# Performance work log

Hardware: AMD Instinct MI355X
Metric: run time of the kernel (lower is better)

The kernel has to match this reference:

```python
import jax, jax.numpy as jnp
import numpy as np

N, V, H, K = 65536, 200, 128, 32

def _corr_cols(a, B):
    # Pearson correlation between vector a [M] and each column of B [M, V]
    ac = a - a.mean()
    Bc = B - B.mean(axis=0)
    num = (ac[:, None] * Bc).sum(axis=0)
    den = jnp.sqrt((ac ** 2).sum() * (Bc ** 2).sum(axis=0))
    return jnp.nan_to_num(num / den, nan=0.0)

def _pairwise_features(tv, ti, cv, ci):
    # tv, ti: [N]; cv, ci: [N, V] -> features [V, 11]
    tvc = tv[:, None]
    both = (1.0 - ti)[:, None] * (1.0 - ci)
    n = both.sum(0) + 1e-8
    tmean = (tvc * both).sum(0) / n
    cmean = (cv * both).sum(0) / n
    tcent = (tvc - tmean) * both
    ccent = (cv - cmean) * both
    cov = (tcent * ccent).sum(0) / n
    tstd = jnp.sqrt((tcent ** 2).sum(0) / n + 1e-8)
    cstd = jnp.sqrt((ccent ** 2).sum(0) / n + 1e-8)
    corr = cov / (tstd * cstd + 1e-8)
    mi = -0.5 * jnp.log(1.0 - jnp.minimum(corr ** 2, 0.99) + 1e-8)
    tmin, tmax = tv.min(), tv.max()
    cmin, cmax = cv.min(0), cv.max(0)
    overlap = jnp.maximum(0.0, (jnp.minimum(tmax, cmax) - jnp.maximum(tmin, cmin)) / (jnp.maximum(tmax - tmin, cmax - cmin) + 1e-8))
    lag = _corr_cols(tv[1:], cv[:-1])       # corrcoef(candidate[:-1], target[1:])
    rev = _corr_cols(tv[:-1], cv[1:])       # corrcoef(target[:-1], candidate[1:])
    var_t = jnp.var(tv)
    coef = corr * jnp.std(tv) / (cv.std(0) + 1e-8)
    residual = tvc - coef * (cv - cv.mean(0))
    var_ratio = residual.var(0) / (var_t + 1e-8)
    intv = (ci > 0.5).astype(tv.dtype)
    t_int = (tvc * intv).sum(0) / (intv.sum(0) + 1e-8)
    t_no = (tvc * (1.0 - intv)).sum(0) / ((1.0 - intv).sum(0) + 1e-8)
    effect = jnp.abs(t_int - t_no)
    tr = jnp.argsort(jnp.argsort(tv)).astype(tv.dtype)
    cr = jnp.argsort(jnp.argsort(cv, axis=0), axis=0).astype(tv.dtype)
    rank_corr = _corr_cols(tr, cr)
    feats = jnp.stack([corr, jnp.abs(corr), corr ** 2, mi, overlap, effect,
                       rank_corr, jnp.sign(corr), lag, rev, var_ratio], axis=-1)
    return jnp.nan_to_num(feats, nan=0.0)

def _forward(target_embedding, node_embeddings, data, W_pair, b_pair, Wq, bq, Wk, bk,
             W1, b1, ln_scale, ln_offset, W2, b2, W3, b3, Wd, target_idx):
    n_vars = node_embeddings.shape[0]
    tv, ti = data[:, target_idx, 0], data[:, target_idx, 1]
    cv, ci = data[:, :, 0], data[:, :, 1]
    pf = _pairwise_features(tv, ti, cv, ci)                       # [V, 11]
    pf = jnp.where((jnp.arange(n_vars) == target_idx)[:, None], 0.0, pf)
    q = target_embedding @ Wq + bq                                # [K]
    k = node_embeddings @ Wk + bk + (pf @ W_pair + b_pair)        # [V, K]
    scores = (k @ q) / jnp.sqrt(jnp.asarray(float(K), dtype=q.dtype))
    te = jnp.broadcast_to(target_embedding, (n_vars, target_embedding.shape[0]))
    combined = jnp.concatenate([te, node_embeddings, pf * 10.0], axis=-1)  # [V, 2H+11]
    h = jax.nn.gelu(combined @ W1 + b1)
    mu = h.mean(-1, keepdims=True)
    var = ((h - mu) ** 2).mean(-1, keepdims=True)
    h = (h - mu) / jnp.sqrt(var + 1e-5) * ln_scale + ln_offset    # LayerNorm (haiku eps=1e-5)
    h = jax.nn.gelu(h @ W2 + b2)
    net = (h @ W3 + b3)[:, 0]
    direct = (pf[:, jnp.array([0, 8, 10])] @ Wd)[:, 0]
    return scores + net + 0.5 * direct

def setup_inputs():
    key = jax.random.key(0)
    ks = jax.random.split(key, 16)
    def vs_uniform(k, fan_in, shape):
        # hk.initializers.VarianceScaling(2.0, 'fan_in', 'uniform')
        lim = np.sqrt(6.0 / fan_in)
        return jax.random.uniform(k, shape, minval=-lim, maxval=lim, dtype=jnp.float32)
    vals = jax.random.normal(ks[0], (N, V), dtype=jnp.float32)
    intv = (jax.random.uniform(ks[1], (N, V)) < 0.1).astype(jnp.float32)
    data = jnp.stack([vals, intv, jnp.ones((N, V), jnp.float32)], axis=-1)  # [N, V, 3]
    return {
        'target_embedding': jax.random.normal(ks[2], (H,), dtype=jnp.float32),
        'node_embeddings': jax.random.normal(ks[3], (V, H), dtype=jnp.float32),
        'data': data,
        'W_pair': vs_uniform(ks[4], 11, (11, K)), 'b_pair': jnp.zeros((K,), jnp.float32),
        'Wq': vs_uniform(ks[5], H, (H, K)), 'bq': jnp.zeros((K,), jnp.float32),
        'Wk': vs_uniform(ks[6], H, (H, K)), 'bk': jnp.zeros((K,), jnp.float32),
        'W1': vs_uniform(ks[7], 2 * H + 11, (2 * H + 11, H)), 'b1': jnp.zeros((H,), jnp.float32),
        'ln_scale': jnp.ones((H,), jnp.float32), 'ln_offset': jnp.zeros((H,), jnp.float32),
        'W2': vs_uniform(ks[8], H, (H, H // 2)), 'b2': jnp.zeros((H // 2,), jnp.float32),
        'W3': vs_uniform(ks[9], H // 2, (H // 2, 1)), 'b3': jnp.zeros((1,), jnp.float32),
        'Wd': vs_uniform(ks[10], 3, (3, 1)),
        'target_idx': 0,
    }

def reference(target_embedding, node_embeddings, data, W_pair, b_pair, Wq, bq, Wk, bk,
              W1, b1, ln_scale, ln_offset, W2, b2, W3, b3, Wd, target_idx):
    return _forward(target_embedding, node_embeddings, data, W_pair, b_pair, Wq, bq, Wk, bk,
                    W1, b1, ln_scale, ln_offset, W2, b2, W3, b3, Wd, target_idx)
```

## Files before the change

### kernel.cpp

```cpp
#include <hip/hip_runtime.h>
#include <stdint.h>

#define N_ROWS 65536
#define NV 200
#define NH 128
#define NKD 32
#define NBKT 32768
#define NB2A 512

__device__ __forceinline__ uint32_t fkey(float x){
  uint32_t u = __float_as_uint(x);
  return (u & 0x80000000u) ? ~u : (u | 0x80000000u);
}

__global__ __launch_bounds__(256) void k_extract(
    const float* __restrict__ data, const int* __restrict__ tgt,
    float* __restrict__ tvArr, float* __restrict__ tiArr,
    unsigned int* __restrict__ histT, double* __restrict__ tvP){
  int i = blockIdx.x*256 + threadIdx.x;
  int tg = *tgt;
  float v  = data[(size_t)i*600 + tg*3 + 0];
  float ti = data[(size_t)i*600 + tg*3 + 1];
  tvArr[i] = v; tiArr[i] = ti;
  atomicAdd(&histT[fkey(v)>>17], 1u);
  double s = (double)v, ss = (double)v*(double)v;
  float mn = v, mx = v;
  for (int off=32; off; off>>=1){
    s  += __shfl_down(s,  off);
    ss += __shfl_down(ss, off);
    mn = fminf(mn, __shfl_down(mn, off));
    mx = fmaxf(mx, __shfl_down(mx, off));
  }
  __shared__ double sd[4][4];
  int w = threadIdx.x >> 6;
  if ((threadIdx.x & 63) == 0){ sd[w][0]=s; sd[w][1]=ss; sd[w][2]=mn; sd[w][3]=mx; }
  __syncthreads();
  if (threadIdx.x == 0){
    double S=0, SS=0, MN=sd[0][2], MX=sd[0][3];
    for (int q=0;q<4;q++){ S+=sd[q][0]; SS+=sd[q][1]; MN=fmin(MN,sd[q][2]); MX=fmax(MX,sd[q][3]); }
    double* p = tvP + (size_t)blockIdx.x*4;
    p[0]=S; p[1]=SS; p[2]=MN; p[3]=MX;
  }
}

__global__ __launch_bounds__(256) void k_comb_tv(const double* __restrict__ tvP,
                                                 double* __restrict__ tvStats){
  int t = threadIdx.x;
  double s = tvP[t*4+0], ss = tvP[t*4+1], mn = tvP[t*4+2], mx = tvP[t*4+3];
  for (int off=32; off; off>>=1){
    s  += __shfl_down(s,  off);
    ss += __shfl_down(ss, off);
    mn = fmin(mn, __shfl_down(mn, off));
    mx = fmax(mx, __shfl_down(mx, off));
  }
  __shared__ double sd[4][4];
  int w = t >> 6;
  if ((t & 63) == 0){ sd[w][0]=s; sd[w][1]=ss; sd[w][2]=mn; sd[w][3]=mx; }
  __syncthreads();
  if (t == 0){
    double S=0, SS=0, MN=sd[0][2], MX=sd[0][3];
    for (int q=0;q<4;q++){ S+=sd[q][0]; SS+=sd[q][1]; MN=fmin(MN,sd[q][2]); MX=fmax(MX,sd[q][3]); }
    tvStats[0]=S; tvStats[1]=SS; tvStats[2]=MN; tvStats[3]=MX;
  }
}

__global__ __launch_bounds__(256) void k_scan(unsigned int* __restrict__ histT){
  int t = threadIdx.x;
  unsigned int s = 0;
  unsigned int loc[128];
  #pragma unroll 8
  for (int k=0;k<128;k++){ loc[k] = histT[t*128+k]; s += loc[k]; }
  __shared__ unsigned int aux[256];
  aux[t] = s; __syncthreads();
  for (int off=1; off<256; off<<=1){
    unsigned int v = (t>=off) ? aux[t-off] : 0u;
    __syncthreads();
    aux[t] += v;
    __syncthreads();
  }
  unsigned int run = aux[t] - s;
  #pragma unroll 8
  for (int k=0;k<128;k++){
    unsigned int c = loc[k];
    float mid = (float)run + 0.5f*((float)c - 1.f);
    histT[t*128+k] = __float_as_uint(mid);
    run += c;
  }
}

__global__ __launch_bounds__(256) void k_trank(const float* __restrict__ tvArr,
                                               const unsigned int* __restrict__ histT,
                                               float* __restrict__ trArr){
  int i = blockIdx.x*256 + threadIdx.x;
  trArr[i] = __uint_as_float(histT[fkey(tvArr[i])>>17]);
}

__global__ __launch_bounds__(256, 2) void k_main(
    const float* __restrict__ data, const float* __restrict__ tvArr,
    const float* __restrict__ tiArr, uint16_t* __restrict__ bktT,
    double* __restrict__ colP, float* __restrict__ colMM){
  __shared__ float   cvS[64][201];
  __shared__ uint8_t ciS[64][204];
  __shared__ float   tvS[66];
  __shared__ float   tiS[64];
  int t = threadIdx.x, blk = blockIdx.x;
  double acc[13];
  #pragma unroll
  for (int s=0;s<13;s++) acc[s]=0.0;
  float cmin = 3.4e38f, cmax = -3.4e38f;

  for (int st=0; st<2; ++st){
    int i0 = blk*128 + st*64;
    const float4* rb = (const float4*)(data + (size_t)i0*600);
    #pragma unroll 2
    for (int k=0;k<38;k++){
      int f = t + k*256;
      if (f < 9600){
        float4 v = rb[f];
        int r  = f/150;
        int e4 = f - r*150;
        int m  = e4 % 3;
        int c0 = (4*e4)/3;
        if (m==0){ cvS[r][c0]=v.x; ciS[r][c0]=(uint8_t)(v.y>0.5f); cvS[r][c0+1]=v.w; }
        else if (m==1){ ciS[r][c0]=(uint8_t)(v.x>0.5f); cvS[r][c0+1]=v.z; ciS[r][c0+1]=(uint8_t)(v.w>0.5f); }
        else { cvS[r][c0+1]=v.y; ciS[r][c0+1]=(uint8_t)(v.z>0.5f); }
      }
    }
    if (t < 66){ int i = i0 - 1 + t; tvS[t] = (i>=0 && i<N_ROWS) ? tvArr[i] : 0.f; }
    else if (t >= 128 && t < 192){ tiS[t-128] = tiArr[i0 + (t-128)]; }
    __syncthreads();
    if (t < NV){
      float facc[13];
      #pragma unroll
      for (int s=0;s<13;s++) facc[s]=0.f;
      for (int r=0;r<64;r++){
        float cv = cvS[r][t];
        float ci = (float)ciS[r][t];
        float tv = tvS[r+1], tvm = tvS[r], tvp = tvS[r+2];
        float ti = tiS[r];
        float b  = (1.f-ti)*(1.f-ci);
        facc[0]+=cv;        facc[1]+=cv*cv;     facc[2]+=tv*cv;
        facc[3]+=ci;        facc[4]+=tv*ci;
        facc[5]+=b;         facc[6]+=tv*b;      facc[7]+=cv*b;
        facc[8]+=tv*cv*b;   facc[9]+=tv*tv*b;   facc[10]+=cv*cv*b;
        facc[11]+=tvp*cv;   facc[12]+=tvm*cv;
        cmin = fminf(cmin, cv); cmax = fmaxf(cmax, cv);
      }
      #pragma unroll
      for (int s=0;s<13;s++) acc[s] += (double)facc[s];
    }
    {
      int r = t & 63, cb = t >> 6;
      for (int cc=cb; cc<NV; cc+=4){
        float cv = cvS[r][cc];
        bktT[(size_t)cc*N_ROWS + i0 + r] = (uint16_t)(fkey(cv)>>17);
      }
    }
    __syncthreads();
  }
  if (t < NV){
    double* dst = colP + ((size_t)t*NB2A + blk)*16;
    #pragma unroll
    for (int s=0;s<13;s++) dst[s] = acc[s];
    float* mm = colMM + ((size_t)t*NB2A + blk)*2;
    mm[0]=cmin; mm[1]=cmax;
  }
}

__global__ __launch_bounds__(64) void k_comb_cols(const double* __restrict__ colP,
                                                  const float* __restrict__ colMM,
                                                  double* __restrict__ colStats){
  int j = blockIdx.x, t = threadIdx.x;
  double a[13];
  #pragma unroll
  for (int s=0;s<13;s++) a[s]=0.0;
  float mn = 3.4e38f, mx = -3.4e38f;
  for (int b=t; b<NB2A; b+=64){
    const double* p = colP + ((size_t)j*NB2A + b)*16;
    #pragma unroll
    for (int s=0;s<13;s++) a[s] += p[s];
    const float* m = colMM + ((size_t)j*NB2A + b)*2;
    mn = fminf(mn, m[0]); mx = fmaxf(mx, m[1]);
  }
  for (int off=32; off; off>>=1){
    #pragma unroll
    for (int s=0;s<13;s++) a[s] += __shfl_down(a[s], off);
    mn = fminf(mn, __shfl_down(mn, off));
    mx = fmaxf(mx, __shfl_down(mx, off));
  }
  if (t == 0){
    double* d = colStats + (size_t)j*16;
    #pragma unroll
    for (int s=0;s<13;s++) d[s] = a[s];
    d[13] = (double)mn; d[14] = (double)mx;
  }
}

__global__ __launch_bounds__(256) void k_rank(const uint16_t* __restrict__ bktT,
                                              const float* __restrict__ trArr,
                                              double* __restrict__ colStats){
  __shared__ unsigned int h[NBKT];
  __shared__ unsigned int aux[256];
  __shared__ double daux[4];
  int t = threadIdx.x, j = blockIdx.x;
  const uint16_t* col = bktT + (size_t)j*N_ROWS;
  for (int k=t; k<NBKT; k+=256) h[k]=0u;
  __syncthreads();
  for (int k=0;k<N_ROWS/256;k++){
    int b = (int)col[t + k*256];
    atomicAdd(&h[b], 1u);
  }
  __syncthreads();
  unsigned int s = 0;
  for (int k=0;k<128;k++) s += h[t*128+k];
  aux[t]=s; __syncthreads();
  for (int off=1; off<256; off<<=1){
    unsigned int v = (t>=off) ? aux[t-off] : 0u;
    __syncthreads();
    aux[t] += v;
    __syncthreads();
  }
  unsigned int run = aux[t] - s;
  for (int k=0;k<128;k++){
    unsigned int c = h[t*128+k];
    float mid = (float)run + 0.5f*((float)c - 1.f);
    h[t*128+k] = __float_as_uint(mid);
    run += c;
  }
  __syncthreads();
  double srr = 0.0;
  for (int k=0;k<N_ROWS/256;k++){
    int i = t + k*256;
    int b = (int)col[i];
    srr += (double)trArr[i] * (double)__uint_as_float(h[b]);
  }
  for (int off=32; off; off>>=1) srr += __shfl_down(srr, off);
  if ((t&63)==0) daux[t>>6] = srr;
  __syncthreads();
  if (t==0) colStats[(size_t)j*16 + 15] = daux[0]+daux[1]+daux[2]+daux[3];
}

__device__ __forceinline__ float gelu_t(float x){
  float x3 = x*x*x;
  return 0.5f*x*(1.f + tanhf(0.7978845608f*(x + 0.044715f*x3)));
}

__global__ __launch_bounds__(128) void k_head(
    const float* __restrict__ te, const float* __restrict__ ne, const float* __restrict__ data,
    const float* __restrict__ Wpair, const float* __restrict__ bpair,
    const float* __restrict__ Wq, const float* __restrict__ bq,
    const float* __restrict__ Wk, const float* __restrict__ bk,
    const float* __restrict__ W1, const float* __restrict__ b1,
    const float* __restrict__ lns, const float* __restrict__ lno,
    const float* __restrict__ W2, const float* __restrict__ b2,
    const float* __restrict__ W3, const float* __restrict__ b3,
    const float* __restrict__ Wd, const int* __restrict__ tgt,
    const double* __restrict__ colStats, const double* __restrict__ tvStats,
    const float* __restrict__ tvArr, float* __restrict__ out){
  int j = blockIdx.x, t = threadIdx.x;
  int tg = *tgt;
  const double* cs = colStats + (size_t)j*16;
  double S_c=cs[0], S_cc=cs[1], S_tc=cs[2], S_ci=cs[3], S_ti=cs[4], S_b=cs[5],
         S_tb=cs[6], S_cb=cs[7], S_tcb=cs[8], S_ttb=cs[9], S_ccb=cs[10], L=cs[11], R=cs[12];
  float cmin=(float)cs[13], cmax=(float)cs[14];
  double S_rr=cs[15];
  double S_t=tvStats[0], S_tt=tvStats[1];
  float tmin=(float)tvStats[2], tmax=(float)tvStats[3];
  float tv0=tvArr[0], tvN=tvArr[N_ROWS-1];
  float cv0=data[j*3], cvN=data[(size_t)(N_ROWS-1)*600 + j*3];
  const double Nd = (double)N_ROWS;
  double n = S_b + 1e-8;
  double tmean=S_tb/n, cmean=S_cb/n;
  double cov=(S_tcb - tmean*S_cb - cmean*S_tb + tmean*cmean*S_b)/n;
  double t2=S_ttb - 2.0*tmean*S_tb + tmean*tmean*S_b;
  double c2=S_ccb - 2.0*cmean*S_cb + cmean*cmean*S_b;
  double tstd=sqrt(t2/n + 1e-8), cstd=sqrt(c2/n + 1e-8);
  double corr = cov/(tstd*cstd + 1e-8);
  double mi = -0.5*log(1.0 - fmin(corr*corr, 0.99) + 1e-8);
  float ovn = fminf(tmax,cmax) - fmaxf(tmin,cmin);
  float ovd = fmaxf(tmax-tmin, cmax-cmin) + 1e-8f;
  float overlap = fmaxf(0.f, ovn/ovd);
  double M = Nd - 1.0;
  double Sa=S_t-(double)tv0, Saa=S_tt-(double)tv0*(double)tv0;
  double Sb2=S_c-(double)cvN, Sbb=S_cc-(double)cvN*(double)cvN;
  double lnum = L - Sa*Sb2/M;
  double lden2 = (Saa - Sa*Sa/M)*(Sbb - Sb2*Sb2/M);
  double lag = (lden2 > 0.0) ? lnum/sqrt(lden2) : 0.0;
  double Sa2=S_t-(double)tvN, Saa2=S_tt-(double)tvN*(double)tvN;
  double Sc2=S_c-(double)cv0, Scc2=S_cc-(double)cv0*(double)cv0;
  double rnum = R - Sa2*Sc2/M;
  double rden2 = (Saa2 - Sa2*Sa2/M)*(Scc2 - Sc2*Sc2/M);
  double rev = (rden2 > 0.0) ? rnum/sqrt(rden2) : 0.0;
  double var_t = S_tt/Nd - (S_t/Nd)*(S_t/Nd);
  double var_c = S_cc/Nd - (S_c/Nd)*(S_c/Nd);
  double coef = corr*sqrt(var_t)/(sqrt(var_c) + 1e-8);
  double covf = S_tc/Nd - (S_t/Nd)*(S_c/Nd);
  double var_res = var_t + coef*coef*var_c - 2.0*coef*covf;
  double var_ratio = var_res/(var_t + 1e-8);
  double t_int = S_ti/(S_ci + 1e-8);
  double t_no  = (S_t - S_ti)/((Nd - S_ci) + 1e-8);
  double effect = fabs(t_int - t_no);
  const double m_ = (Nd-1.0)*0.5;
  double rank_corr = (S_rr - Nd*m_*m_) / (Nd*(Nd*Nd-1.0)/12.0);
  float pf[11];
  pf[0]=(float)corr; pf[1]=(float)fabs(corr); pf[2]=(float)(corr*corr); pf[3]=(float)mi;
  pf[4]=overlap; pf[5]=(float)effect; pf[6]=(float)rank_corr;
  pf[7]=(float)((corr>0.0)-(corr<0.0)); pf[8]=(float)lag; pf[9]=(float)rev; pf[10]=(float)var_ratio;
  if (j == tg){
    #pragma unroll
    for (int q=0;q<11;q++) pf[q]=0.f;
  }
  const float* nej = ne + (size_t)j*NH;
  float h = b1[t];
  for (int e=0;e<NH;e++) h += te[e]*W1[e*NH + t];
  for (int e=0;e<NH;e++) h += nej[e]*W1[(NH+e)*NH + t];
  #pragma unroll
  for (int f=0;f<11;f++) h += 10.f*pf[f]*W1[(2*NH+f)*NH + t];
  h = gelu_t(h);
  __shared__ float redW[2];
  __shared__ float hnS[NH];
  __shared__ float h2S[64];
  float v = h;
  for (int off=32; off; off>>=1) v += __shfl_down(v, off);
  if ((t&63)==0) redW[t>>6]=v;
  __syncthreads();
  float mu = (redW[0]+redW[1])*(1.f/128.f);
  __syncthreads();
  float d = h - mu;
  v = d*d;
  for (int off=32; off; off>>=1) v += __shfl_down(v, off);
  if ((t&63)==0) redW[t>>6]=v;
  __syncthreads();
  float var = (redW[0]+redW[1])*(1.f/128.f);
  float hn = d/sqrtf(var + 1e-5f)*lns[t] + lno[t];
  hnS[t] = hn;
  __syncthreads();
  if (t < 64){
    float h2 = b2[t];
    for (int o=0;o<NH;o++) h2 += hnS[o]*W2[o*64 + t];
    h2S[t] = gelu_t(h2);
  }
  __syncthreads();
  float netv = 0.f, scv = 0.f;
  if (t < 64){
    float v2 = h2S[t]*W3[t];
    for (int off=32; off; off>>=1) v2 += __shfl_down(v2, off);
    if (t==0) netv = v2 + b3[0];
  }
  if (t < 32){
    float q = bq[t], k = bk[t] + bpair[t];
    for (int e=0;e<NH;e++){ q += te[e]*Wq[e*NKD + t]; k += nej[e]*Wk[e*NKD + t]; }
    #pragma unroll
    for (int f=0;f<11;f++) k += pf[f]*Wpair[f*NKD + t];
    float sc = k*q;
    for (int off=16; off; off>>=1) sc += __shfl_down(sc, off, 32);
    if (t==0) scv = sc/sqrtf(32.f);
  }
  if (t == 0){
    float direct = pf[0]*Wd[0] + pf[8]*Wd[1] + pf[10]*Wd[2];
    out[j] = scv + netv + 0.5f*direct;
  }
}

extern "C" void kernel_launch(void* const* d_in, const int* in_sizes, int n_in,
                              void* d_out, int out_size, void* d_ws, size_t ws_size,
                              hipStream_t stream) {
  const float* te    = (const float*)d_in[0];
  const float* ne    = (const float*)d_in[1];
  const float* data  = (const float*)d_in[2];
  const float* Wpair = (const float*)d_in[3];
  const float* bpair = (const float*)d_in[4];
  const float* Wq    = (const float*)d_in[5];
  const float* bq    = (const float*)d_in[6];
  const float* Wk    = (const float*)d_in[7];
  const float* bk    = (const float*)d_in[8];
  const float* W1    = (const float*)d_in[9];
  const float* b1    = (const float*)d_in[10];
  const float* lns   = (const float*)d_in[11];
  const float* lno   = (const float*)d_in[12];
  const float* W2    = (const float*)d_in[13];
  const float* b2    = (const float*)d_in[14];
  const float* W3    = (const float*)d_in[15];
  const float* b3    = (const float*)d_in[16];
  const float* Wd    = (const float*)d_in[17];
  const int*   tgt   = (const int*)d_in[18];
  float* out = (float*)d_out;

  char* ws = (char*)d_ws;
  size_t off = 0;
  auto alloc = [&](size_t bytes)->char*{
    char* p = ws + off;
    off = (off + bytes + 255) & ~(size_t)255;
    return p;
  };
  uint16_t*     bktT     = (uint16_t*)    alloc((size_t)NV*N_ROWS*2);
  float*        tvArr    = (float*)       alloc(N_ROWS*4);
  float*        tiArr    = (float*)       alloc(N_ROWS*4);
  float*        trArr    = (float*)       alloc(N_ROWS*4);
  unsigned int* histT    = (unsigned int*)alloc(NBKT*4);
  double*       tvP      = (double*)      alloc(256*4*8);
  double*       tvStats  = (double*)      alloc(4*8);
  double*       colP     = (double*)      alloc((size_t)NV*NB2A*16*8);
  float*        colMM    = (float*)       alloc((size_t)NV*NB2A*2*4);
  double*       colStats = (double*)      alloc((size_t)NV*16*8);
  if (off > ws_size) return;

  hipMemsetAsync(histT, 0, NBKT*4, stream);
  k_extract<<<dim3(N_ROWS/256), dim3(256), 0, stream>>>(data, tgt, tvArr, tiArr, histT, tvP);
  k_comb_tv<<<dim3(1), dim3(256), 0, stream>>>(tvP, tvStats);
  k_scan<<<dim3(1), dim3(256), 0, stream>>>(histT);
  k_trank<<<dim3(N_ROWS/256), dim3(256), 0, stream>>>(tvArr, histT, trArr);
  k_main<<<dim3(NB2A), dim3(256), 0, stream>>>(data, tvArr, tiArr, bktT, colP, colMM);
  k_comb_cols<<<dim3(NV), dim3(64), 0, stream>>>(colP, colMM, colStats);
  k_rank<<<dim3(NV), dim3(256), 0, stream>>>(bktT, trArr, colStats);
  k_head<<<dim3(NV), dim3(128), 0, stream>>>(te, ne, data, Wpair, bpair, Wq, bq, Wk, bk,
                                             W1, b1, lns, lno, W2, b2, W3, b3, Wd, tgt,
                                             colStats, tvStats, tvArr, out);
}
```

Before: 463.8 us.

## Shrink k_main stage tiles, widen rank/comb blocks, stage scan histogram in LDS

k_main now stages 32 rows per step instead of 64, which roughly halves LDS use, and requests 4 blocks per CU instead of 2 to raise occupancy. Per-block column partials are stored as floats, with min and max packed into the same record, which removes a separate buffer and halves the partial traffic. k_comb_cols uses 256 threads with a shared-memory cross-wave reduction. k_rank uses 512 threads with a padded histogram layout to reduce LDS bank conflicts, and k_scan stages the histogram through padded LDS instead of a per-thread register array. Storing partial sums as float risks some loss of precision, and the larger per-block LDS in k_rank limits it to one block per CU.

```diff
diff --git a/kernel.cpp b/kernel.cpp
--- a/kernel.cpp
+++ b/kernel.cpp
@@ -7,6 +7,7 @@
 #define NKD 32
 #define NBKT 32768
 #define NB2A 512
+#define ROWS_ST 32
 
 __device__ __forceinline__ uint32_t fkey(float x){
   uint32_t u = __float_as_uint(x);
@@ -65,12 +66,14 @@
 }
 
 __global__ __launch_bounds__(256) void k_scan(unsigned int* __restrict__ histT){
+  __shared__ unsigned int h[256*129];
+  __shared__ unsigned int aux[256];
   int t = threadIdx.x;
+  for (int idx=t; idx<NBKT; idx+=256) h[(idx>>7)*129 + (idx&127)] = histT[idx];
+  __syncthreads();
   unsigned int s = 0;
-  unsigned int loc[128];
   #pragma unroll 8
-  for (int k=0;k<128;k++){ loc[k] = histT[t*128+k]; s += loc[k]; }
-  __shared__ unsigned int aux[256];
+  for (int k=0;k<128;k++) s += h[t*129+k];
   aux[t] = s; __syncthreads();
   for (int off=1; off<256; off<<=1){
     unsigned int v = (t>=off) ? aux[t-off] : 0u;
@@ -81,11 +84,12 @@
   unsigned int run = aux[t] - s;
   #pragma unroll 8
   for (int k=0;k<128;k++){
-    unsigned int c = loc[k];
-    float mid = (float)run + 0.5f*((float)c - 1.f);
-    histT[t*128+k] = __float_as_uint(mid);
+    unsigned int c = h[t*129+k];
+    h[t*129+k] = __float_as_uint((float)run + 0.5f*((float)c - 1.f));
     run += c;
   }
+  __syncthreads();
+  for (int idx=t; idx<NBKT; idx+=256) histT[idx] = h[(idx>>7)*129 + (idx&127)];
 }
 
 __global__ __launch_bounds__(256) void k_trank(const float* __restrict__ tvArr,
@@ -95,27 +99,27 @@
   trArr[i] = __uint_as_float(histT[fkey(tvArr[i])>>17]);
 }
 
-__global__ __launch_bounds__(256, 2) void k_main(
+__global__ __launch_bounds__(256, 4) void k_main(
     const float* __restrict__ data, const float* __restrict__ tvArr,
     const float* __restrict__ tiArr, uint16_t* __restrict__ bktT,
-    double* __restrict__ colP, float* __restrict__ colMM){
-  __shared__ float   cvS[64][201];
-  __shared__ uint8_t ciS[64][204];
-  __shared__ float   tvS[66];
-  __shared__ float   tiS[64];
+    float* __restrict__ colP){
+  __shared__ float   cvS[ROWS_ST][201];
+  __shared__ uint8_t ciS[ROWS_ST][204];
+  __shared__ float   tvS[ROWS_ST+2];
+  __shared__ float   tiS[ROWS_ST];
   int t = threadIdx.x, blk = blockIdx.x;
   double acc[13];
   #pragma unroll
   for (int s=0;s<13;s++) acc[s]=0.0;
   float cmin = 3.4e38f, cmax = -3.4e38f;
 
-  for (int st=0; st<2; ++st){
-    int i0 = blk*128 + st*64;
+  for (int st=0; st<4; ++st){
+    int i0 = blk*128 + st*ROWS_ST;
     const float4* rb = (const float4*)(data + (size_t)i0*600);
     #pragma unroll 2
-    for (int k=0;k<38;k++){
+    for (int k=0;k<19;k++){
       int f = t + k*256;
-      if (f < 9600){
+      if (f < 4800){
         float4 v = rb[f];
         int r  = f/150;
         int e4 = f - r*150;
@@ -126,14 +130,14 @@
         else { cvS[r][c0+1]=v.y; ciS[r][c0+1]=(uint8_t)(v.z>0.5f); }
       }
     }
-    if (t < 66){ int i = i0 - 1 + t; tvS[t] = (i>=0 && i<N_ROWS) ? tvArr[i] : 0.f; }
-    else if (t >= 128 && t < 192){ tiS[t-128] = tiArr[i0 + (t-128)]; }
+    if (t < ROWS_ST+2){ int i = i0 - 1 + t; tvS[t] = (i>=0 && i<N_ROWS) ? tvArr[i] : 0.f; }
+    else if (t >= 64 && t < 64+ROWS_ST){ tiS[t-64] = tiArr[i0 + (t-64)]; }
     __syncthreads();
     if (t < NV){
       float facc[13];
       #pragma unroll
       for (int s=0;s<13;s++) facc[s]=0.f;
-      for (int r=0;r<64;r++){
+      for (int r=0;r<ROWS_ST;r++){
         float cv = cvS[r][t];
         float ci = (float)ciS[r][t];
         float tv = tvS[r+1], tvm = tvS[r], tvp = tvS[r+2];
@@ -150,8 +154,8 @@
       for (int s=0;s<13;s++) acc[s] += (double)facc[s];
     }
     {
-      int r = t & 63, cb = t >> 6;
-      for (int cc=cb; cc<NV; cc+=4){
+      int r = t & 31, cb = t >> 5;
+      for (int cc=cb; cc<NV; cc+=8){
         float cv = cvS[r][cc];
         bktT[(size_t)cc*N_ROWS + i0 + r] = (uint16_t)(fkey(cv)>>17);
       }
@@ -159,28 +163,25 @@
     __syncthreads();
   }
   if (t < NV){
-    double* dst = colP + ((size_t)t*NB2A + blk)*16;
-    #pragma unroll
-    for (int s=0;s<13;s++) dst[s] = acc[s];
-    float* mm = colMM + ((size_t)t*NB2A + blk)*2;
-    mm[0]=cmin; mm[1]=cmax;
-  }
-}
-
-__global__ __launch_bounds__(64) void k_comb_cols(const double* __restrict__ colP,
-                                                  const float* __restrict__ colMM,
-                                                  double* __restrict__ colStats){
+    float* dst = colP + ((size_t)t*NB2A + blk)*16;
+    #pragma unroll
+    for (int s=0;s<13;s++) dst[s] = (float)acc[s];
+    dst[13]=cmin; dst[14]=cmax;
+  }
+}
+
+__global__ __launch_bounds__(256) void k_comb_cols(const float* __restrict__ colP,
+                                                   double* __restrict__ colStats){
   int j = blockIdx.x, t = threadIdx.x;
   double a[13];
   #pragma unroll
   for (int s=0;s<13;s++) a[s]=0.0;
   float mn = 3.4e38f, mx = -3.4e38f;
-  for (int b=t; b<NB2A; b+=64){
-    const double* p = colP + ((size_t)j*NB2A + b)*16;
-    #pragma unroll
-    for (int s=0;s<13;s++) a[s] += p[s];
-    const float* m = colMM + ((size_t)j*NB2A + b)*2;
-    mn = fminf(mn, m[0]); mx = fmaxf(mx, m[1]);
+  for (int b=t; b<NB2A; b+=256){
+    const float* p = colP + ((size_t)j*NB2A + b)*16;
+    #pragma unroll
+    for (int s=0;s<13;s++) a[s] += (double)p[s];
+    mn = fminf(mn, p[13]); mx = fmaxf(mx, p[14]);
   }
   for (int off=32; off; off>>=1){
     #pragma unroll
@@ -188,56 +189,71 @@
     mn = fminf(mn, __shfl_down(mn, off));
     mx = fmaxf(mx, __shfl_down(mx, off));
   }
+  __shared__ double sd[4][15];
+  int w = t >> 6;
+  if ((t & 63) == 0){
+    #pragma unroll
+    for (int s=0;s<13;s++) sd[w][s]=a[s];
+    sd[w][13]=(double)mn; sd[w][14]=(double)mx;
+  }
+  __syncthreads();
   if (t == 0){
     double* d = colStats + (size_t)j*16;
     #pragma unroll
-    for (int s=0;s<13;s++) d[s] = a[s];
-    d[13] = (double)mn; d[14] = (double)mx;
-  }
-}
-
-__global__ __launch_bounds__(256) void k_rank(const uint16_t* __restrict__ bktT,
-                                              const float* __restrict__ trArr,
-                                              double* __restrict__ colStats){
-  __shared__ unsigned int h[NBKT];
-  __shared__ unsigned int aux[256];
-  __shared__ double daux[4];
+    for (int s=0;s<13;s++) d[s] = sd[0][s]+sd[1][s]+sd[2][s]+sd[3][s];
+    double MN=sd[0][13], MX=sd[0][14];
+    for (int q=1;q<4;q++){ MN=fmin(MN,sd[q][13]); MX=fmax(MX,sd[q][14]); }
+    d[13]=MN; d[14]=MX;
+  }
+}
+
+__global__ __launch_bounds__(512, 1) void k_rank(const uint16_t* __restrict__ bktT,
+                                                 const float* __restrict__ trArr,
+                                                 double* __restrict__ colStats){
+  __shared__ unsigned int h[512*65];
+  __shared__ unsigned int aux[512];
+  __shared__ double daux[8];
   int t = threadIdx.x, j = blockIdx.x;
   const uint16_t* col = bktT + (size_t)j*N_ROWS;
-  for (int k=t; k<NBKT; k+=256) h[k]=0u;
-  __syncthreads();
-  for (int k=0;k<N_ROWS/256;k++){
-    int b = (int)col[t + k*256];
-    atomicAdd(&h[b], 1u);
+  for (int idx=t; idx<512*65; idx+=512) h[idx]=0u;
+  __syncthreads();
+  for (int k=0;k<N_ROWS/512;k++){
+    int b = (int)col[t + k*512];
+    atomicAdd(&h[(b>>6)*65 + (b&63)], 1u);
   }
   __syncthreads();
   unsigned int s = 0;
-  for (int k=0;k<128;k++) s += h[t*128+k];
+  #pragma unroll 8
+  for (int k=0;k<64;k++) s += h[t*65+k];
   aux[t]=s; __syncthreads();
-  for (int off=1; off<256; off<<=1){
+  for (int off=1; off<512; off<<=1){
     unsigned int v = (t>=off) ? aux[t-off] : 0u;
     __syncthreads();
     aux[t] += v;
     __syncthreads();
   }
   unsigned int run = aux[t] - s;
-  for (int k=0;k<128;k++){
-    unsigned int c = h[t*128+k];
-    float mid = (float)run + 0.5f*((float)c - 1.f);
-    h[t*128+k] = __float_as_uint(mid);
+  #pragma unroll 8
+  for (int k=0;k<64;k++){
+    unsigned int c = h[t*65+k];
+    h[t*65+k] = __float_as_uint((float)run + 0.5f*((float)c - 1.f));
     run += c;
   }
   __syncthreads();
   double srr = 0.0;
-  for (int k=0;k<N_ROWS/256;k++){
-    int i = t + k*256;
+  for (int k=0;k<N_ROWS/512;k++){
+    int i = t + k*512;
     int b = (int)col[i];
-    srr += (double)trArr[i] * (double)__uint_as_float(h[b]);
+    srr += (double)trArr[i] * (double)__uint_as_float(h[(b>>6)*65 + (b&63)]);
   }
   for (int off=32; off; off>>=1) srr += __shfl_down(srr, off);
   if ((t&63)==0) daux[t>>6] = srr;
   __syncthreads();
-  if (t==0) colStats[(size_t)j*16 + 15] = daux[0]+daux[1]+daux[2]+daux[3];
+  if (t==0){
+    double s8=0;
+    for (int q=0;q<8;q++) s8 += daux[q];
+    colStats[(size_t)j*16 + 15] = s8;
+  }
 }
 
 __device__ __forceinline__ float gelu_t(float x){
@@ -400,8 +416,7 @@
   unsigned int* histT    = (unsigned int*)alloc(NBKT*4);
   double*       tvP      = (double*)      alloc(256*4*8);
   double*       tvStats  = (double*)      alloc(4*8);
-  double*       colP     = (double*)      alloc((size_t)NV*NB2A*16*8);
-  float*        colMM    = (float*)       alloc((size_t)NV*NB2A*2*4);
+  float*        colP     = (float*)       alloc((size_t)NV*NB2A*16*4);
   double*       colStats = (double*)      alloc((size_t)NV*16*8);
   if (off > ws_size) return;
 
@@ -410,9 +425,9 @@
   k_comb_tv<<<dim3(1), dim3(256), 0, stream>>>(tvP, tvStats);
   k_scan<<<dim3(1), dim3(256), 0, stream>>>(histT);
   k_trank<<<dim3(N_ROWS/256), dim3(256), 0, stream>>>(tvArr, histT, trArr);
-  k_main<<<dim3(NB2A), dim3(256), 0, stream>>>(data, tvArr, tiArr, bktT, colP, colMM);
-  k_comb_cols<<<dim3(NV), dim3(64), 0, stream>>>(colP, colMM, colStats);
-  k_rank<<<dim3(NV), dim3(256), 0, stream>>>(bktT, trArr, colStats);
+  k_main<<<dim3(NB2A), dim3(256), 0, stream>>>(data, tvArr, tiArr, bktT, colP);
+  k_comb_cols<<<dim3(NV), dim3(256), 0, stream>>>(colP, colStats);
+  k_rank<<<dim3(NV), dim3(512), 0, stream>>>(bktT, trArr, colStats);
   k_head<<<dim3(NV), dim3(128), 0, stream>>>(te, ne, data, Wpair, bpair, Wq, bq, Wk, bk,
                                              W1, b1, lns, lno, W2, b2, W3, b3, Wd, tgt,
                                              colStats, tvStats, tvArr, out);
```

Result: faster. 419.3 us (-9.6%).
